# Optimization experiments

Hardware: AMD Instinct MI355X
Metric: run time of the kernel (lower is better)

The kernel has to match this reference:

```python
import jax, jax.numpy as jnp
import numpy as np

B, TA, TV, D, H = 4, 1024, 1024, 512, 8
HD = D // H
SCALE = HD ** -0.5
LN_EPS = 1e-5


def setup_inputs() -> dict:
    key = jax.random.key(0)
    ks = jax.random.split(key, 16)
    init = lambda k, shape, s: (jax.random.normal(k, shape, jnp.float32) * s)
    inp = {
        'q': jax.random.normal(ks[0], (B, TA, D), jnp.float32),
        'k': jax.random.normal(ks[1], (B, TV, D), jnp.float32),
        'v': jax.random.normal(ks[2], (B, TV, D), jnp.float32),
        'guide_map': jax.random.uniform(ks[3], (B, TA, TV), jnp.float32),
        'Wq': init(ks[4], (D, D), D ** -0.5), 'bq': jnp.zeros((D,), jnp.float32),
        'Wk': init(ks[5], (D, D), D ** -0.5), 'bk': jnp.zeros((D,), jnp.float32),
        'Wv': init(ks[6], (D, D), D ** -0.5), 'bv': jnp.zeros((D,), jnp.float32),
        'Wo': init(ks[7], (D, D), D ** -0.5), 'bo': jnp.zeros((D,), jnp.float32),
        'ln_gamma': jnp.ones((D,), jnp.float32),
        'ln_beta': jnp.zeros((D,), jnp.float32),
        'gate': jnp.zeros((1,), jnp.float32),
        'bias_scale': jnp.array(10.0, jnp.float32),
    }
    return inp


def layer_norm(x, gamma, beta):
    mu = jnp.mean(x, axis=-1, keepdims=True)
    var = jnp.mean(jnp.square(x - mu), axis=-1, keepdims=True)
    return (x - mu) * jax.lax.rsqrt(var + LN_EPS) * gamma + beta


def reference(q, k, v, guide_map, Wq, bq, Wk, bk, Wv, bv, Wo, bo, ln_gamma, ln_beta, gate, bias_scale):
    # project and split heads: [B, H, T, hd]
    Q = (q @ Wq.T + bq).reshape(B, TA, H, HD).transpose(0, 2, 1, 3)
    K = (k @ Wk.T + bk).reshape(B, TV, H, HD).transpose(0, 2, 1, 3)
    V = (v @ Wv.T + bv).reshape(B, TV, H, HD).transpose(0, 2, 1, 3)
    scores = jnp.einsum('bhqd,bhkd->bhqk', Q, K) * SCALE
    # transport bias, broadcast over heads (guide_map is [B,Ta,Tv])
    transport_bias = jnp.log(guide_map + 1e-8) * jax.nn.softplus(bias_scale)
    scores = scores + transport_bias[:, None, :, :]
    attn = jax.nn.softmax(scores, axis=-1)  # dropout is identity in eval
    context = jnp.einsum('bhqk,bhkd->bhqd', attn, V)
    context = context.transpose(0, 2, 1, 3).reshape(B, TA, D)
    out = context @ Wo.T + bo
    return layer_norm(q + jax.nn.sigmoid(gate) * out, ln_gamma, ln_beta)
```

## Files before the change

kernel.cpp:

```cpp
#include <hip/hip_runtime.h>
#include <hip/hip_bf16.h>
#include <math.h>

typedef __bf16 bf16_t;
typedef _Float16 hf16_t;
typedef bf16_t bf16x8 __attribute__((ext_vector_type(8)));
typedef bf16_t bf16x4 __attribute__((ext_vector_type(4)));
typedef hf16_t hf16x8 __attribute__((ext_vector_type(8)));
typedef float f32x4 __attribute__((ext_vector_type(4)));
typedef short s16x4 __attribute__((ext_vector_type(4)));

#define B_  4
#define TA_ 1024
#define TV_ 1024
#define D_  512
#define H_  8
#define HD_ 64
#define SCALE_ 0.125f

__device__ inline void g2l16(const void* g, void* l) {
    __builtin_amdgcn_global_load_lds(
        (const __attribute__((address_space(1))) void*)g,
        (__attribute__((address_space(3))) void*)l, 16, 0, 0);
}

__device__ inline f32x4 mfma16_bf16(bf16x4 a, bf16x4 b, f32x4 c) {
    return __builtin_amdgcn_mfma_f32_16x16x16bf16_1k(
        __builtin_bit_cast(s16x4, a), __builtin_bit_cast(s16x4, b), c, 0, 0, 0);
}

__global__ __launch_bounds__(256) void prep_all(
    const float* __restrict__ G, hf16_t* __restrict__ bias_t,
    const float* __restrict__ q, const float* __restrict__ k, const float* __restrict__ v,
    const float* __restrict__ Wq, const float* __restrict__ Wk,
    const float* __restrict__ Wv, const float* __restrict__ Wo,
    bf16_t* __restrict__ qb, bf16_t* __restrict__ kb, bf16_t* __restrict__ vb,
    bf16_t* __restrict__ Wb)
{
    const int tid = threadIdx.x;
    if (blockIdx.x < 1024) {
        __shared__ float Gt[64][68];
        const int kt = blockIdx.x & 15, q64 = (blockIdx.x >> 4) & 15, b = blockIdx.x >> 8;
        const int row = tid >> 4, col4 = (tid & 15) * 4;
        #pragma unroll
        for (int it = 0; it < 4; ++it) {
            int r = it * 16 + row;
            f32x4 g = *(const f32x4*)(G + ((size_t)(b * TA_ + q64 * 64 + r)) * TV_ + kt * 64 + col4);
            *(f32x4*)&Gt[r][col4] = g;
        }
        __syncthreads();
        const int lane = tid & 63, wave = tid >> 6, quad = lane >> 4, l16 = lane & 15;
        hf16x8 lo, hi;
        #pragma unroll
        for (int ct = 0; ct < 4; ++ct) {
            #pragma unroll
            for (int r = 0; r < 4; ++r) {
                float gv = Gt[wave * 16 + l16][ct * 16 + quad * 4 + r];
                float lb = __logf(gv + 1e-8f);
                int idx = ct * 4 + r;
                if (idx < 8) lo[idx] = (hf16_t)lb; else hi[idx - 8] = (hf16_t)lb;
            }
        }
        size_t doff = ((((size_t)b * 16 + kt) * 16 + q64) * 256 + tid) * 16;
        *(hf16x8*)(bias_t + doff) = lo;
        *(hf16x8*)(bias_t + doff + 8) = hi;
    } else {
        const size_t i = ((size_t)(blockIdx.x - 1024) * 256 + tid) * 8;
        const float* src; bf16_t* dst; size_t off;
        const size_t M2 = (size_t)1 << 21;
        if (i < M2)          { src = q; dst = qb; off = i; }
        else if (i < 2 * M2) { src = k; dst = kb; off = i - M2; }
        else if (i < 3 * M2) { src = v; dst = vb; off = i - 2 * M2; }
        else {
            size_t j = i - 3 * M2;
            int wsel = (int)(j >> 18); off = j & 262143;
            src = (wsel == 0) ? Wq : (wsel == 1) ? Wk : (wsel == 2) ? Wv : Wo;
            dst = Wb + ((size_t)wsel << 18);
        }
        f32x4 a = *(const f32x4*)(src + off), c = *(const f32x4*)(src + off + 4);
        bf16x8 r;
        #pragma unroll
        for (int t = 0; t < 4; ++t) { r[t] = (bf16_t)a[t]; r[t + 4] = (bf16_t)c[t]; }
        *(bf16x8*)(dst + off) = r;
    }
}

__device__ inline void gemm128_core(
    const bf16_t* __restrict__ X, const bf16_t* __restrict__ W,
    int mbase, int nbase, bf16_t (*__restrict__ Asm)[128 * 32],
    bf16_t (*__restrict__ Bsm)[128 * 32], f32x4 acc[4][4])
{
    const int tid  = threadIdx.x;
    const int wave = tid >> 6, lane = tid & 63;
    const int quad = lane >> 4, l16 = lane & 15;
    const int wm = wave & 1, wn = wave >> 1;
    const int srow = lane >> 2;
    const int scol = (lane & 3) * 8;

    auto stage = [&](int kt, int buf) {
        const int k0 = kt * 32;
        #pragma unroll
        for (int i = 0; i < 2; ++i) {
            const int row = wave * 32 + i * 16;
            g2l16(X + (size_t)(mbase + row + srow) * D_ + k0 + scol,
                  &Asm[buf][row * 32] + (size_t)lane * 8);
            g2l16(W + (size_t)(nbase + row + srow) * D_ + k0 + scol,
                  &Bsm[buf][row * 32] + (size_t)lane * 8);
        }
    };

    stage(0, 0);
    __syncthreads();
    for (int kt = 0; kt < 16; ++kt) {
        const int buf = kt & 1;
        if (kt < 15) stage(kt + 1, buf ^ 1);
        bf16x8 af[4], bf_[4];
        #pragma unroll
        for (int t = 0; t < 4; ++t) {
            af[t]  = *(const bf16x8*)&Asm[buf][(wm * 64 + t * 16 + l16) * 32 + quad * 8];
            bf_[t] = *(const bf16x8*)&Bsm[buf][(wn * 64 + t * 16 + l16) * 32 + quad * 8];
        }
        #pragma unroll
        for (int mt = 0; mt < 4; ++mt) {
            #pragma unroll
            for (int nt = 0; nt < 4; ++nt)
                acc[mt][nt] = __builtin_amdgcn_mfma_f32_16x16x32_bf16(af[mt], bf_[nt], acc[mt][nt], 0, 0, 0);
        }
        __syncthreads();
    }
}

__global__ __launch_bounds__(256) void gemm_qkv(
    const bf16_t* __restrict__ qb, const bf16_t* __restrict__ kb, const bf16_t* __restrict__ vb,
    const bf16_t* __restrict__ Wb,
    const float* __restrict__ bq, const float* __restrict__ bk, const float* __restrict__ bv,
    bf16_t* __restrict__ Qp, bf16_t* __restrict__ Kp, bf16_t* __restrict__ Vt)
{
    __shared__ bf16_t Asm[2][128 * 32];
    __shared__ bf16_t Bsm[2][128 * 32];

    const int tid  = threadIdx.x;
    const int wave = tid >> 6, lane = tid & 63;
    const int quad = lane >> 4, l16 = lane & 15;
    const int wm = wave & 1, wn = wave >> 1;
    const int mbase = blockIdx.x * 128, nbase = blockIdx.y * 128;
    const int z = blockIdx.z;

    const bf16_t* X   = (z == 0) ? qb : (z == 1) ? kb : vb;
    const float* bias = (z == 0) ? bq : (z == 1) ? bk : bv;
    const bf16_t* W   = Wb + ((size_t)z << 18);

    f32x4 acc[4][4] = {};
    gemm128_core(X, W, mbase, nbase, Asm, Bsm, acc);

    bf16_t* out = (z == 0) ? Qp : (z == 1) ? Kp : Vt;
    #pragma unroll
    for (int mt = 0; mt < 4; ++mt) {
        #pragma unroll
        for (int nt = 0; nt < 4; ++nt) {
            #pragma unroll
            for (int r = 0; r < 4; ++r) {
                int m = mbase + wm * 64 + mt * 16 + quad * 4 + r;
                int n = nbase + wn * 64 + nt * 16 + l16;
                float val = acc[mt][nt][r] + bias[n];
                int b = m >> 10, t = m & 1023, h = n >> 6, hd = n & 63;
                if (z != 2)
                    out[(((size_t)(b * H_ + h) * TA_) + t) * HD_ + hd] = (bf16_t)val;
                else
                    out[((size_t)(b * H_ + h) * HD_ + hd) * TV_ + t] = (bf16_t)val;
            }
        }
    }
}

__global__ __launch_bounds__(256) void gemm_out(
    const bf16_t* __restrict__ ctx, const bf16_t* __restrict__ Wob,
    const float* __restrict__ bo, bf16_t* __restrict__ op)
{
    __shared__ bf16_t Asm[2][128 * 32];
    __shared__ bf16_t Bsm[2][128 * 32];

    const int tid  = threadIdx.x;
    const int wave = tid >> 6, lane = tid & 63;
    const int quad = lane >> 4, l16 = lane & 15;
    const int wm = wave & 1, wn = wave >> 1;
    const int mbase = blockIdx.x * 128, nbase = blockIdx.y * 128;

    f32x4 acc[4][4] = {};
    gemm128_core(ctx, Wob, mbase, nbase, Asm, Bsm, acc);

    #pragma unroll
    for (int mt = 0; mt < 4; ++mt) {
        #pragma unroll
        for (int nt = 0; nt < 4; ++nt) {
            #pragma unroll
            for (int r = 0; r < 4; ++r) {
                int m = mbase + wm * 64 + mt * 16 + quad * 4 + r;
                int n = nbase + wn * 64 + nt * 16 + l16;
                op[(size_t)m * D_ + n] = (bf16_t)(acc[mt][nt][r] + bo[n]);
            }
        }
    }
}

__global__ __launch_bounds__(256) void attn_kernel(
    const bf16_t* __restrict__ Qp, const bf16_t* __restrict__ Kp,
    const bf16_t* __restrict__ Vt, const hf16_t* __restrict__ bias_t,
    const float* __restrict__ bias_scale,
    bf16_t* __restrict__ Opart, float* __restrict__ mpart, float* __restrict__ lpart)
{
    __shared__ bf16_t Ksm[2][64][72];
    __shared__ bf16_t Vsm[2][64][72];

    const int tid  = threadIdx.x;
    const int wave = tid >> 6, lane = tid & 63;
    const int quad = lane >> 4, l16 = lane & 15;
    const int bh = blockIdx.x, b = bh >> 3;
    const int q64 = blockIdx.y;
    const int z = blockIdx.z;
    const int t0 = z * 8;
    const int qbase = q64 * 64 + wave * 16;
    const int rsub = lane >> 3, csub = lane & 7;
    const int shsrc = (lane & 48) | ((lane >> 2) & 12);

    const float sp = log1pf(__expf(bias_scale[0]));

    bf16x8 aq[2];
    #pragma unroll
    for (int s = 0; s < 2; ++s)
        aq[s] = *(const bf16x8*)(Qp + ((size_t)bh * TA_ + qbase + l16) * HD_ + s * 32 + quad * 8);

    f32x4 o[4] = {};
    float m_ = -1e30f, l_ = 0.f;

    auto issue_kv = [&](int kt, bf16x8 kr[2], bf16x8 vr[2]) {
        const int kbase = kt * 64;
        #pragma unroll
        for (int i = 0; i < 2; ++i) {
            int row = wave * 16 + i * 8 + rsub;
            kr[i] = *(const bf16x8*)(Kp + ((size_t)bh * TV_ + kbase + row) * HD_ + csub * 8);
            vr[i] = *(const bf16x8*)(Vt + ((size_t)bh * HD_ + row) * TV_ + kbase + csub * 8);
        }
    };
    auto write_kv = [&](int buf, bf16x8 kr[2], bf16x8 vr[2]) {
        #pragma unroll
        for (int i = 0; i < 2; ++i) {
            int row = wave * 16 + i * 8 + rsub;
            *(bf16x8*)&Ksm[buf][row][csub * 8] = kr[i];
            *(bf16x8*)&Vsm[buf][row][csub * 8] = vr[i];
        }
    };

    const hf16_t* bias_base = bias_t + (((size_t)b * 16 * 16 + q64) * 256 + tid) * 16;
    auto bias_ld = [&](int kt, hf16x8& lo, hf16x8& hi) {
        const hf16_t* bp = bias_base + (size_t)kt * 65536;
        lo = *(const hf16x8*)bp;
        hi = *(const hf16x8*)(bp + 8);
    };
    hf16x8 b0lo, b0hi, b1lo, b1hi;
    bias_ld(t0, b0lo, b0hi);
    bias_ld(t0 + 1, b1lo, b1hi);

    {
        bf16x8 kr[2], vr[2];
        issue_kv(t0, kr, vr);
        write_kv(0, kr, vr);
    }
    __syncthreads();

    auto tile_body = [&](int lk, int buf, hf16x8& slo, hf16x8& shi) {
        const int kt = t0 + lk;
        bf16x8 krn[2], vrn[2];
        if (lk < 7) issue_kv(kt + 1, krn, vrn);
        hf16x8 clo = slo, chi = shi;
        if (lk < 6) bias_ld(kt + 2, slo, shi);

        f32x4 st[4];
        #pragma unroll
        for (int ct = 0; ct < 4; ++ct) {
            f32x4 acc = {};
            #pragma unroll
            for (int s = 0; s < 2; ++s) {
                bf16x8 bk = *(const bf16x8*)&Ksm[buf][ct * 16 + l16][s * 32 + quad * 8];
                acc = __builtin_amdgcn_mfma_f32_16x16x32_bf16(bk, aq[s], acc, 0, 0, 0);
            }
            st[ct] = acc;
        }
        float sv[4][4], mx = -1e30f;
        #pragma unroll
        for (int ct = 0; ct < 4; ++ct) {
            #pragma unroll
            for (int r = 0; r < 4; ++r) {
                int idx = ct * 4 + r;
                float lb = (idx < 8) ? (float)clo[idx] : (float)chi[idx - 8];
                float val = fmaf(lb, sp, st[ct][r] * SCALE_);
                sv[ct][r] = val;
                mx = fmaxf(mx, val);
            }
        }
        mx = fmaxf(mx, __shfl_xor(mx, 16, 64));
        mx = fmaxf(mx, __shfl_xor(mx, 32, 64));
        float mn = fmaxf(m_, mx);
        float alpha = __expf(m_ - mn);
        m_ = mn;
        float ls = 0.f;
        #pragma unroll
        for (int ct = 0; ct < 4; ++ct) {
            #pragma unroll
            for (int r = 0; r < 4; ++r) {
                float p = __expf(sv[ct][r] - mn);
                sv[ct][r] = p;
                ls += p;
            }
        }
        ls += __shfl_xor(ls, 16, 64);
        ls += __shfl_xor(ls, 32, 64);
        l_ = l_ * alpha + ls;
        #pragma unroll
        for (int r = 0; r < 4; ++r) {
            float af = __shfl(alpha, shsrc | r, 64);
            #pragma unroll
            for (int dt = 0; dt < 4; ++dt) o[dt][r] *= af;
        }
        #pragma unroll
        for (int ct = 0; ct < 4; ++ct) {
            bf16x4 ap;
            #pragma unroll
            for (int r = 0; r < 4; ++r) ap[r] = (bf16_t)sv[ct][r];
            #pragma unroll
            for (int dt = 0; dt < 4; ++dt) {
                bf16x4 bv = *(const bf16x4*)&Vsm[buf][dt * 16 + l16][ct * 16 + quad * 4];
                o[dt] = mfma16_bf16(ap, bv, o[dt]);
            }
        }
        if (lk < 7) write_kv(buf ^ 1, krn, vrn);
        __syncthreads();
    };

    #pragma unroll 1
    for (int kk = 0; kk < 8; kk += 2) {
        tile_body(kk,     0, b0lo, b0hi);
        tile_body(kk + 1, 1, b1lo, b1hi);
    }

    const size_t blk = (size_t)bh * 16 + q64;
    bf16x8 plo, phi;
    #pragma unroll
    for (int dt = 0; dt < 4; ++dt) {
        #pragma unroll
        for (int r = 0; r < 4; ++r) {
            int idx = dt * 4 + r;
            if (idx < 8) plo[idx] = (bf16_t)o[dt][r]; else phi[idx - 8] = (bf16_t)o[dt][r];
        }
    }
    size_t poff = (((size_t)z * 512 + blk) * 256 + tid) * 16;
    *(bf16x8*)(Opart + poff) = plo;
    *(bf16x8*)(Opart + poff + 8) = phi;
    if (quad == 0) {
        int row = wave * 16 + l16;
        mpart[((size_t)z * 512 + blk) * 64 + row] = m_;
        lpart[((size_t)z * 512 + blk) * 64 + row] = l_;
    }
}

__global__ __launch_bounds__(256) void attn_combine(
    const bf16_t* __restrict__ Opart, const float* __restrict__ mpart,
    const float* __restrict__ lpart, bf16_t* __restrict__ ctx)
{
    const int tid  = threadIdx.x;
    const int wave = tid >> 6, lane = tid & 63;
    const int quad = lane >> 4, l16 = lane & 15;
    const int bh = blockIdx.x, b = bh >> 3, h = bh & 7;
    const int q64 = blockIdx.y;
    const size_t blk = (size_t)bh * 16 + q64;

    size_t p0 = (blk * 256 + tid) * 16;
    size_t p1 = (((size_t)512 + blk) * 256 + tid) * 16;
    bf16x8 a0 = *(const bf16x8*)(Opart + p0), a1 = *(const bf16x8*)(Opart + p0 + 8);
    bf16x8 c0 = *(const bf16x8*)(Opart + p1), c1 = *(const bf16x8*)(Opart + p1 + 8);

    float s0[4], s1[4];
    #pragma unroll
    for (int r = 0; r < 4; ++r) {
        int row = wave * 16 + quad * 4 + r;
        float m0 = mpart[blk * 64 + row], m1 = mpart[(512 + blk) * 64 + row];
        float l0 = lpart[blk * 64 + row], l1 = lpart[(512 + blk) * 64 + row];
        float mm = fmaxf(m0, m1);
        float e0 = __expf(m0 - mm), e1 = __expf(m1 - mm);
        float L = l0 * e0 + l1 * e1;
        s0[r] = e0 / L; s1[r] = e1 / L;
    }
    #pragma unroll
    for (int dt = 0; dt < 4; ++dt) {
        #pragma unroll
        for (int r = 0; r < 4; ++r) {
            int idx = dt * 4 + r;
            float v0 = (idx < 8) ? (float)a0[idx] : (float)a1[idx - 8];
            float v1 = (idx < 8) ? (float)c0[idx] : (float)c1[idx - 8];
            float v = v0 * s0[r] + v1 * s1[r];
            int qrow = q64 * 64 + wave * 16 + quad * 4 + r;
            ctx[((size_t)b * TA_ + qrow) * D_ + h * HD_ + dt * 16 + l16] = (bf16_t)v;
        }
    }
}

__global__ __launch_bounds__(256) void ln_kernel(
    const float* __restrict__ q, const bf16_t* __restrict__ outp,
    const float* __restrict__ gamma, const float* __restrict__ beta,
    const float* __restrict__ gate, float* __restrict__ y)
{
    const int row = blockIdx.x, tid = threadIdx.x;
    const float sg = 1.f / (1.f + __expf(-gate[0]));
    const size_t base = (size_t)row * D_;
    float x0 = q[base + tid]       + sg * (float)outp[base + tid];
    float x1 = q[base + tid + 256] + sg * (float)outp[base + tid + 256];
    float s = x0 + x1, sq = x0 * x0 + x1 * x1;
    #pragma unroll
    for (int off = 1; off < 64; off <<= 1) {
        s  += __shfl_xor(s,  off, 64);
        sq += __shfl_xor(sq, off, 64);
    }
    __shared__ float ss[4], sqq[4];
    if ((tid & 63) == 0) { ss[tid >> 6] = s; sqq[tid >> 6] = sq; }
    __syncthreads();
    s  = ss[0] + ss[1] + ss[2] + ss[3];
    sq = sqq[0] + sqq[1] + sqq[2] + sqq[3];
    const float mu = s * (1.f / D_);
    const float var = sq * (1.f / D_) - mu * mu;
    const float rstd = rsqrtf(var + 1e-5f);
    y[base + tid]       = (x0 - mu) * rstd * gamma[tid] + beta[tid];
    y[base + tid + 256] = (x1 - mu) * rstd * gamma[tid + 256] + beta[tid + 256];
}

extern "C" void kernel_launch(void* const* d_in, const int* in_sizes, int n_in,
                              void* d_out, int out_size, void* d_ws, size_t ws_size,
                              hipStream_t stream) {
    const float* q       = (const float*)d_in[0];
    const float* k       = (const float*)d_in[1];
    const float* v       = (const float*)d_in[2];
    const float* guide   = (const float*)d_in[3];
    const float* Wq      = (const float*)d_in[4];
    const float* bq      = (const float*)d_in[5];
    const float* Wk      = (const float*)d_in[6];
    const float* bk      = (const float*)d_in[7];
    const float* Wv      = (const float*)d_in[8];
    const float* bv      = (const float*)d_in[9];
    const float* Wo      = (const float*)d_in[10];
    const float* bo      = (const float*)d_in[11];
    const float* gamma   = (const float*)d_in[12];
    const float* beta    = (const float*)d_in[13];
    const float* gate    = (const float*)d_in[14];
    const float* bscale  = (const float*)d_in[15];

    char* w = (char*)d_ws;
    bf16_t* qb     = (bf16_t*)(w);
    bf16_t* kb     = (bf16_t*)(w + (4u  << 20));
    bf16_t* vb     = (bf16_t*)(w + (8u  << 20));
    bf16_t* Wb     = (bf16_t*)(w + (12u << 20));
    bf16_t* Qp     = (bf16_t*)(w + (14u << 20));
    bf16_t* Kp     = (bf16_t*)(w + (18u << 20));
    bf16_t* Vt     = (bf16_t*)(w + (22u << 20));
    bf16_t* ctx    = (bf16_t*)(w + (26u << 20));
    hf16_t* bias_t = (hf16_t*)(w + (30u << 20));
    bf16_t* Opart  = (bf16_t*)(w + (38u << 20));
    float*  mpart  = (float*) (w + (46u << 20));
    float*  lpart  = (float*) (w + (47u << 20));
    bf16_t* op     = (bf16_t*)(w);

    prep_all<<<4608, 256, 0, stream>>>(guide, bias_t, q, k, v, Wq, Wk, Wv, Wo, qb, kb, vb, Wb);
    gemm_qkv<<<dim3(32, 4, 3), 256, 0, stream>>>(qb, kb, vb, Wb, bq, bk, bv, Qp, Kp, Vt);
    attn_kernel<<<dim3(32, 16, 2), 256, 0, stream>>>(Qp, Kp, Vt, bias_t, bscale, Opart, mpart, lpart);
    attn_combine<<<dim3(32, 16), 256, 0, stream>>>(Opart, mpart, lpart, ctx);
    gemm_out<<<dim3(32, 4), 256, 0, stream>>>(ctx, Wb + ((size_t)3 << 18), bo, op);
    ln_kernel<<<4096, 256, 0, stream>>>(q, op, gamma, beta, gate, (float*)d_out);
}
```

Measured before the change: 181.9 us.

## Fuse split-KV attention halves into one 512-thread block with LDS combine

The attention kernel now runs both KV halves inside one 512-thread block, with each group of four waves handling one half. The two partial results are merged through shared memory at the end, which removes the separate combine kernel and the global round trip of partial outputs and softmax statistics. The cost is a larger block with doubled LDS buffers and half as many blocks launched, which may lower occupancy and adds an extra block-wide barrier.

Result: faster. 178.2 us (-2.0%).

```diff
diff --git a/kernel.cpp b/kernel.cpp
--- a/kernel.cpp
+++ b/kernel.cpp
@@ -203,23 +203,22 @@
     }
 }
 
-__global__ __launch_bounds__(256) void attn_kernel(
+__global__ __launch_bounds__(512, 4) void attn_kernel(
     const bf16_t* __restrict__ Qp, const bf16_t* __restrict__ Kp,
     const bf16_t* __restrict__ Vt, const hf16_t* __restrict__ bias_t,
-    const float* __restrict__ bias_scale,
-    bf16_t* __restrict__ Opart, float* __restrict__ mpart, float* __restrict__ lpart)
-{
-    __shared__ bf16_t Ksm[2][64][72];
-    __shared__ bf16_t Vsm[2][64][72];
+    const float* __restrict__ bias_scale, bf16_t* __restrict__ ctx)
+{
+    __shared__ bf16_t Ksm[2][2][64][72];
+    __shared__ bf16_t Vsm[2][2][64][72];
 
     const int tid  = threadIdx.x;
     const int wave = tid >> 6, lane = tid & 63;
+    const int half = wave >> 2, w4 = wave & 3;
     const int quad = lane >> 4, l16 = lane & 15;
-    const int bh = blockIdx.x, b = bh >> 3;
+    const int bh = blockIdx.x, b = bh >> 3, h = bh & 7;
     const int q64 = blockIdx.y;
-    const int z = blockIdx.z;
-    const int t0 = z * 8;
-    const int qbase = q64 * 64 + wave * 16;
+    const int t0 = half * 8;
+    const int qbase = q64 * 64 + w4 * 16;
     const int rsub = lane >> 3, csub = lane & 7;
     const int shsrc = (lane & 48) | ((lane >> 2) & 12);
 
@@ -237,7 +236,7 @@
         const int kbase = kt * 64;
         #pragma unroll
         for (int i = 0; i < 2; ++i) {
-            int row = wave * 16 + i * 8 + rsub;
+            int row = w4 * 16 + i * 8 + rsub;
             kr[i] = *(const bf16x8*)(Kp + ((size_t)bh * TV_ + kbase + row) * HD_ + csub * 8);
             vr[i] = *(const bf16x8*)(Vt + ((size_t)bh * HD_ + row) * TV_ + kbase + csub * 8);
         }
@@ -245,13 +244,14 @@
     auto write_kv = [&](int buf, bf16x8 kr[2], bf16x8 vr[2]) {
         #pragma unroll
         for (int i = 0; i < 2; ++i) {
-            int row = wave * 16 + i * 8 + rsub;
-            *(bf16x8*)&Ksm[buf][row][csub * 8] = kr[i];
-            *(bf16x8*)&Vsm[buf][row][csub * 8] = vr[i];
+            int row = w4 * 16 + i * 8 + rsub;
+            *(bf16x8*)&Ksm[half][buf][row][csub * 8] = kr[i];
+            *(bf16x8*)&Vsm[half][buf][row][csub * 8] = vr[i];
         }
     };
 
-    const hf16_t* bias_base = bias_t + (((size_t)b * 16 * 16 + q64) * 256 + tid) * 16;
+    const int tidb = (w4 << 6) | lane;
+    const hf16_t* bias_base = bias_t + (((size_t)b * 16 * 16 + q64) * 256 + tidb) * 16;
     auto bias_ld = [&](int kt, hf16x8& lo, hf16x8& hi) {
         const hf16_t* bp = bias_base + (size_t)kt * 65536;
         lo = *(const hf16x8*)bp;
@@ -281,7 +281,7 @@
             f32x4 acc = {};
             #pragma unroll
             for (int s = 0; s < 2; ++s) {
-                bf16x8 bk = *(const bf16x8*)&Ksm[buf][ct * 16 + l16][s * 32 + quad * 8];
+                bf16x8 bk = *(const bf16x8*)&Ksm[half][buf][ct * 16 + l16][s * 32 + quad * 8];
                 acc = __builtin_amdgcn_mfma_f32_16x16x32_bf16(bk, aq[s], acc, 0, 0, 0);
             }
             st[ct] = acc;
@@ -329,7 +329,7 @@
             for (int r = 0; r < 4; ++r) ap[r] = (bf16_t)sv[ct][r];
             #pragma unroll
             for (int dt = 0; dt < 4; ++dt) {
-                bf16x4 bv = *(const bf16x4*)&Vsm[buf][dt * 16 + l16][ct * 16 + quad * 4];
+                bf16x4 bv = *(const bf16x4*)&Vsm[half][buf][dt * 16 + l16][ct * 16 + quad * 4];
                 o[dt] = mfma16_bf16(ap, bv, o[dt]);
             }
         }
@@ -343,63 +343,39 @@
         tile_body(kk + 1, 1, b1lo, b1hi);
     }
 
-    const size_t blk = (size_t)bh * 16 + q64;
-    bf16x8 plo, phi;
-    #pragma unroll
-    for (int dt = 0; dt < 4; ++dt) {
+    float* cb = (float*)&Ksm[0][0][0][0];
+    if (half == 1) {
+        float* p = cb + (size_t)tidb * 18;
+        #pragma unroll
+        for (int dt = 0; dt < 4; ++dt) {
+            #pragma unroll
+            for (int r = 0; r < 4; ++r) p[dt * 4 + r] = o[dt][r];
+        }
+        p[16] = m_; p[17] = l_;
+    }
+    __syncthreads();
+    if (half == 0) {
+        const float* p = cb + (size_t)tidb * 18;
+        float s0[4], s1[4];
         #pragma unroll
         for (int r = 0; r < 4; ++r) {
-            int idx = dt * 4 + r;
-            if (idx < 8) plo[idx] = (bf16_t)o[dt][r]; else phi[idx - 8] = (bf16_t)o[dt][r];
-        }
-    }
-    size_t poff = (((size_t)z * 512 + blk) * 256 + tid) * 16;
-    *(bf16x8*)(Opart + poff) = plo;
-    *(bf16x8*)(Opart + poff + 8) = phi;
-    if (quad == 0) {
-        int row = wave * 16 + l16;
-        mpart[((size_t)z * 512 + blk) * 64 + row] = m_;
-        lpart[((size_t)z * 512 + blk) * 64 + row] = l_;
-    }
-}
-
-__global__ __launch_bounds__(256) void attn_combine(
-    const bf16_t* __restrict__ Opart, const float* __restrict__ mpart,
-    const float* __restrict__ lpart, bf16_t* __restrict__ ctx)
-{
-    const int tid  = threadIdx.x;
-    const int wave = tid >> 6, lane = tid & 63;
-    const int quad = lane >> 4, l16 = lane & 15;
-    const int bh = blockIdx.x, b = bh >> 3, h = bh & 7;
-    const int q64 = blockIdx.y;
-    const size_t blk = (size_t)bh * 16 + q64;
-
-    size_t p0 = (blk * 256 + tid) * 16;
-    size_t p1 = (((size_t)512 + blk) * 256 + tid) * 16;
-    bf16x8 a0 = *(const bf16x8*)(Opart + p0), a1 = *(const bf16x8*)(Opart + p0 + 8);
-    bf16x8 c0 = *(const bf16x8*)(Opart + p1), c1 = *(const bf16x8*)(Opart + p1 + 8);
-
-    float s0[4], s1[4];
-    #pragma unroll
-    for (int r = 0; r < 4; ++r) {
-        int row = wave * 16 + quad * 4 + r;
-        float m0 = mpart[blk * 64 + row], m1 = mpart[(512 + blk) * 64 + row];
-        float l0 = lpart[blk * 64 + row], l1 = lpart[(512 + blk) * 64 + row];
-        float mm = fmaxf(m0, m1);
-        float e0 = __expf(m0 - mm), e1 = __expf(m1 - mm);
-        float L = l0 * e0 + l1 * e1;
-        s0[r] = e0 / L; s1[r] = e1 / L;
-    }
-    #pragma unroll
-    for (int dt = 0; dt < 4; ++dt) {
-        #pragma unroll
-        for (int r = 0; r < 4; ++r) {
-            int idx = dt * 4 + r;
-            float v0 = (idx < 8) ? (float)a0[idx] : (float)a1[idx - 8];
-            float v1 = (idx < 8) ? (float)c0[idx] : (float)c1[idx - 8];
-            float v = v0 * s0[r] + v1 * s1[r];
-            int qrow = q64 * 64 + wave * 16 + quad * 4 + r;
-            ctx[((size_t)b * TA_ + qrow) * D_ + h * HD_ + dt * 16 + l16] = (bf16_t)v;
+            float m0 = __shfl(m_, shsrc | r, 64);
+            float l0 = __shfl(l_, shsrc | r, 64);
+            const float* pr = cb + (size_t)((w4 << 6) | (shsrc | r)) * 18;
+            float m1 = pr[16], l1 = pr[17];
+            float mm = fmaxf(m0, m1);
+            float e0 = __expf(m0 - mm), e1 = __expf(m1 - mm);
+            float L = l0 * e0 + l1 * e1;
+            s0[r] = e0 / L; s1[r] = e1 / L;
+        }
+        #pragma unroll
+        for (int dt = 0; dt < 4; ++dt) {
+            #pragma unroll
+            for (int r = 0; r < 4; ++r) {
+                float v = o[dt][r] * s0[r] + p[dt * 4 + r] * s1[r];
+                int qrow = q64 * 64 + w4 * 16 + quad * 4 + r;
+                ctx[((size_t)b * TA_ + qrow) * D_ + h * HD_ + dt * 16 + l16] = (bf16_t)v;
+            }
         }
     }
 }
@@ -462,15 +438,11 @@
     bf16_t* Vt     = (bf16_t*)(w + (22u << 20));
     bf16_t* ctx    = (bf16_t*)(w + (26u << 20));
     hf16_t* bias_t = (hf16_t*)(w + (30u << 20));
-    bf16_t* Opart  = (bf16_t*)(w + (38u << 20));
-    float*  mpart  = (float*) (w + (46u << 20));
-    float*  lpart  = (float*) (w + (47u << 20));
     bf16_t* op     = (bf16_t*)(w);
 
     prep_all<<<4608, 256, 0, stream>>>(guide, bias_t, q, k, v, Wq, Wk, Wv, Wo, qb, kb, vb, Wb);
     gemm_qkv<<<dim3(32, 4, 3), 256, 0, stream>>>(qb, kb, vb, Wb, bq, bk, bv, Qp, Kp, Vt);
-    attn_kernel<<<dim3(32, 16, 2), 256, 0, stream>>>(Qp, Kp, Vt, bias_t, bscale, Opart, mpart, lpart);
-    attn_combine<<<dim3(32, 16), 256, 0, stream>>>(Opart, mpart, lpart, ctx);
+    attn_kernel<<<dim3(32, 16), 512, 0, stream>>>(Qp, Kp, Vt, bias_t, bscale, ctx);
     gemm_out<<<dim3(32, 4), 256, 0, stream>>>(ctx, Wb + ((size_t)3 << 18), bo, op);
     ln_kernel<<<4096, 256, 0, stream>>>(q, op, gamma, beta, gate, (float*)d_out);
 }
```
